# Kernel optimization log

Hardware: AMD Instinct MI355X
Metric: run time of the kernel (lower is better)

Reference implementation:

```python
import jax, jax.numpy as jnp
import numpy as np

H = 512      # hidden_size
GH = 512     # global_hidden_size
V = 128      # VOCAB_SIZE (one-hot arg_hot width)
D = 14       # tree depth; complete binary tree
NUM_OPS = 36
N_INT = 5    # num_internal_ops
N_NODES = 2 ** (D + 1) - 1  # 32767, heap layout: node i has children 2i+1, 2i+2


def _p(key, i, shape, s=0.05):
    return jax.random.normal(jax.random.fold_in(key, i), shape, dtype=jnp.float32) * s


def setup_inputs() -> dict:
    key = jax.random.key(0)
    return {
        "tokens": jax.random.randint(jax.random.fold_in(key, 0), (N_NODES,), 0, V),
        "validity_mask": jnp.ones((NUM_OPS,), jnp.float32),
        # binary tree-LSTM (blstm): 2 children
        "W_iou_b": _p(key, 1, (V, 3 * H)), "U_iou_b": _p(key, 2, (2, H, 3 * H)), "b_iou_b": jnp.zeros((3 * H,), jnp.float32),
        "Wf_b": _p(key, 3, (V, H)), "Uf_b": _p(key, 4, (2, H, H)), "bf_b": jnp.ones((H,), jnp.float32),
        # ternary tree-LSTM (tlstm): 3 children
        "W_iou_t": _p(key, 5, (V, 3 * H)), "U_iou_t": _p(key, 6, (3, H, 3 * H)), "b_iou_t": jnp.zeros((3 * H,), jnp.float32),
        "Wf_t": _p(key, 7, (V, H)), "Uf_t": _p(key, 8, (3, H, H)), "bf_t": jnp.ones((H,), jnp.float32),
        # FFN: one h-by-h layer (ffn_complexity = h^2 * n_layers, n_layers=1)
        "ffn_W": _p(key, 9, (H, H)), "ffn_b": jnp.zeros((H,), jnp.float32),
        # global LSTM (1 layer, 1 step), torch gate order i,f,g,o
        "lstm_Wx": _p(key, 10, (H, 4 * GH)), "lstm_Wh": _p(key, 11, (GH, 4 * GH)), "lstm_b": jnp.zeros((4 * GH,), jnp.float32),
        # actor heads on concat(root_hidden, h_glob)
        "hl_W": _p(key, 12, (H + GH, 2)), "hl_b": jnp.zeros((2,), jnp.float32),
        "int_W": _p(key, 13, (H + GH, N_INT)), "int_b": jnp.zeros((N_INT,), jnp.float32),
        "act_W": _p(key, 14, (H + GH, NUM_OPS)), "act_b": jnp.zeros((NUM_OPS,), jnp.float32),
    }


def _nary_cell(x, hk, ck, W_iou, U_iou, b_iou, Wf, Uf, bf):
    # x: [n, V]; hk, ck: [n, K, H]  (K children)
    iou = x @ W_iou + jnp.einsum('nkh,khg->ng', hk, U_iou) + b_iou
    i, o, u = jnp.split(iou, 3, axis=-1)
    f = jax.nn.sigmoid((x @ Wf + bf)[:, None, :] + jnp.einsum('nkh,khg->nkg', hk, Uf))
    c = jax.nn.sigmoid(i) * jnp.tanh(u) + jnp.sum(f * ck, axis=1)
    h = jax.nn.sigmoid(o) * jnp.tanh(c)
    return h, c


def _forward(tokens, validity_mask, W_iou_b, U_iou_b, b_iou_b, Wf_b, Uf_b, bf_b,
             W_iou_t, U_iou_t, b_iou_t, Wf_t, Uf_t, bf_t, ffn_W, ffn_b,
             lstm_Wx, lstm_Wh, lstm_b, hl_W, hl_b, int_W, int_b, act_W, act_b):
    arg_hot = jax.nn.one_hot(tokens, V, dtype=jnp.float32)  # [N_NODES, V]
    h_prev = c_prev = None
    h_ab = c_ab = None
    # apply_binary_lstm over the whole tree, bottom-up, one batched cell per level
    for lvl in range(D, -1, -1):
        n = 2 ** lvl
        x = arg_hot[n - 1:2 * n - 1]  # level lvl occupies heap slots [2^l-1, 2^{l+1}-2]
        if h_prev is None:
            hk = jnp.zeros((n, 2, H), jnp.float32)  # leaves: tz children
            ck = hk
        else:
            hk = h_prev.reshape(n, 2, H)
            ck = c_prev.reshape(n, 2, H)
        h_prev, c_prev = _nary_cell(x, hk, ck, W_iou_b, U_iou_b, b_iou_b, Wf_b, Uf_b, bf_b)
        if lvl == 1:
            h_ab, c_ab = h_prev, c_prev  # root's children a, b
    # apply_ternary_lstm at depth 0: children = (self.hidden, a.hidden, b.hidden)
    hk3 = jnp.concatenate([h_prev, h_ab], axis=0)[None]  # [1, 3, H]
    ck3 = jnp.concatenate([c_prev, c_ab], axis=0)[None]
    h_root, c_root = _nary_cell(arg_hot[0:1], hk3, ck3, W_iou_t, U_iou_t, b_iou_t, Wf_t, Uf_t, bf_t)
    # apply_ffn (1 layer) then apply_global_lstm (single step from zero state)
    h_f = jnp.maximum(h_root @ ffn_W + ffn_b, 0.0)  # [1, H]
    h_g = jnp.zeros((1, GH), jnp.float32)
    c_g = h_g
    gates = h_f @ lstm_Wx + h_g @ lstm_Wh + lstm_b
    gi, gf, gg, go = jnp.split(gates, 4, axis=-1)
    c_g = jax.nn.sigmoid(gf) * c_g + jax.nn.sigmoid(gi) * jnp.tanh(gg)
    h_g = jax.nn.sigmoid(go) * jnp.tanh(c_g)
    # actor heads
    feat = jnp.concatenate([h_f, h_g], axis=-1)  # [1, H+GH]
    hl = feat @ hl_W + hl_b
    il = feat @ int_W + int_b
    el = jnp.log(validity_mask)[None, :] + feat @ (act_W * validity_mask[None, :]) + act_b * validity_mask
    return jnp.concatenate([hl, il, el], axis=-1)  # [1, 2 + N_INT + NUM_OPS]


def reference(tokens, validity_mask, W_iou_b, U_iou_b, b_iou_b, Wf_b, Uf_b, bf_b,
              W_iou_t, U_iou_t, b_iou_t, Wf_t, Uf_t, bf_t, ffn_W, ffn_b,
              lstm_Wx, lstm_Wh, lstm_b, hl_W, hl_b, int_W, int_b, act_W, act_b):
    return _forward(tokens, validity_mask, W_iou_b, U_iou_b, b_iou_b, Wf_b, Uf_b, bf_b,
                    W_iou_t, U_iou_t, b_iou_t, Wf_t, Uf_t, bf_t, ffn_W, ffn_b,
                    lstm_Wx, lstm_Wh, lstm_b, hl_W, hl_b, int_W, int_b, act_W, act_b)
```

## Files before the change

kernel.cpp:

```cpp
#include <hip/hip_runtime.h>
#include <hip/hip_bf16.h>
#include <math.h>

#define H 512
#define V 128
#define NLEAF 16384

typedef __attribute__((ext_vector_type(4))) float f32x4;
typedef __attribute__((ext_vector_type(8))) short s16x8;
typedef __attribute__((ext_vector_type(4))) unsigned short u16x4;
typedef unsigned short ushort_t;

__device__ ushort_t g_hb0[NLEAF * H];
__device__ ushort_t g_hb1[(NLEAF / 2) * H];
__device__ float    g_c0[NLEAF * H];
__device__ float    g_c1[(NLEAF / 2) * H];
__device__ ushort_t g_UiouT[3 * H * 2 * H];
__device__ ushort_t g_UfT[H * 2 * H];
__device__ ushort_t g_UiouTt[3 * H * 3 * H];
__device__ ushort_t g_UfTt[H * 3 * H];
__device__ float    g_rpart[3 * 3072];
__device__ float    g_root[2 * H];
__device__ float    g_hf[H];
__device__ float    g_gates[4 * H];

__device__ __forceinline__ float sigm(float x) { return 1.0f / (1.0f + __expf(-x)); }
__device__ __forceinline__ float ftanh(float x) {
  return 1.0f - 2.0f / (__expf(2.0f * x) + 1.0f);
}
__device__ __forceinline__ ushort_t f2bf(float x) {
  __hip_bfloat16 b = __float2bfloat16(x);
  return *reinterpret_cast<ushort_t*>(&b);
}
__device__ __forceinline__ float bf2f(ushort_t u) {
  union { unsigned int i; float f; } v; v.i = ((unsigned int)u) << 16; return v.f;
}
__device__ __forceinline__ void gload_lds16(const void* g, void* l) {
  __builtin_amdgcn_global_load_lds(
      (const __attribute__((address_space(1))) unsigned int*)g,
      (__attribute__((address_space(3))) unsigned int*)l, 16, 0, 0);
}

__global__ __launch_bounds__(256) void k_transp(const float* __restrict__ src,
                                                ushort_t* __restrict__ dst,
                                                int R, int Cc) {
  __shared__ float t[32][33];
  int bc = blockIdx.x * 32, br = blockIdx.y * 32;
  int tx = threadIdx.x & 31, ty = threadIdx.x >> 5;
  for (int rr = ty; rr < 32; rr += 8)
    t[rr][tx] = src[(size_t)(br + rr) * Cc + bc + tx];
  __syncthreads();
  for (int rr = ty; rr < 32; rr += 8)
    dst[(size_t)(bc + rr) * R + br + tx] = f2bf(t[tx][rr]);
}

__global__ __launch_bounds__(256) void k_leaf(const int* __restrict__ tokens,
                                              const float* __restrict__ Wiou,
                                              const float* __restrict__ biou) {
  const int total = NLEAF * 128;
  for (int q = blockIdx.x * 256 + threadIdx.x; q < total; q += gridDim.x * 256) {
    int i = q >> 7, jv = q & 127;
    int tok = tokens[(NLEAF - 1) + i];
    const f32x4* Wr = (const f32x4*)(Wiou + (size_t)tok * 1536);
    const f32x4* bv = (const f32x4*)biou;
    f32x4 wi = Wr[jv] + bv[jv];
    f32x4 wo = Wr[128 + jv] + bv[128 + jv];
    f32x4 wu = Wr[256 + jv] + bv[256 + jv];
    u16x4 hv; f32x4 cv;
    #pragma unroll
    for (int r = 0; r < 4; ++r) {
      float c = sigm(wi[r]) * ftanh(wu[r]);
      float h = sigm(wo[r]) * ftanh(c);
      cv[r] = c;
      hv[r] = f2bf(h);
    }
    *reinterpret_cast<u16x4*>(&g_hb0[(size_t)q * 4]) = hv;
    *reinterpret_cast<f32x4*>(&g_c0[(size_t)q * 4]) = cv;
  }
}

__global__ __launch_bounds__(128, 2) void k_mfma_lvl(int lvl,
    const int* __restrict__ tokens,
    const float* __restrict__ Wiou, const float* __restrict__ biou,
    const float* __restrict__ Wf, const float* __restrict__ bf) {
  const int n = 1 << lvl;
  const int node0 = n - 1;
  const int outp = lvl & 1;
  const ushort_t* __restrict__ hprev = outp ? g_hb0 : g_hb1;
  const float* __restrict__ cprev = outp ? g_c0 : g_c1;
  ushort_t* __restrict__ hout = outp ? g_hb1 : g_hb0;
  float* __restrict__ cout = outp ? g_c1 : g_c0;

  const int i0 = blockIdx.x * 64;
  const int j0 = blockIdx.y * 64;
  const int tid = threadIdx.x;
  const int lane = tid & 63;
  const int w = tid >> 6;

  __shared__ f32x4 smemv[2560];
  char* smem = (char*)smemv;

  const char* gp[10];
  unsigned lb[10], lstr[10];
  {
    int kb = (lane >> 4) * 16;
    #pragma unroll
    for (int q = 0; q < 10; ++q) {
      int c = w * 10 + q;
      if (c < 4) {
        int row = i0 + c * 16 + (lane & 15);
        gp[q] = (const char*)hprev + (size_t)row * 2048 + kb;
        lb[q] = c * 1024u;
        lstr[q] = 4096u;
      } else {
        int ct = c - 4;
        int col = ct * 16 + (lane & 15);
        int g = col >> 6, jj = j0 + (col & 63);
        const ushort_t* Ub = (g < 3) ? (g_UiouT + (size_t)(g * 512 + jj) * 1024)
                                     : (g_UfT + (size_t)jj * 1024);
        gp[q] = (const char*)Ub + kb;
        lb[q] = 8192u + ct * 1024u;
        lstr[q] = 16384u;
      }
    }
  }

#define STAGE(BUF)                                                     \
  {                                                                    \
    _Pragma("unroll")                                                  \
    for (int q = 0; q < 10; ++q) {                                     \
      gload_lds16(gp[q], smem + lb[q] + (unsigned)(BUF) * lstr[q]);    \
      gp[q] += 64;                                                     \
    }                                                                  \
  }

  f32x4 acc[4][10];
  #pragma unroll
  for (int a = 0; a < 4; ++a)
    #pragma unroll
    for (int b = 0; b < 10; ++b) acc[a][b] = (f32x4){0.f, 0.f, 0.f, 0.f};

#define COMPUTE(FA)                                                          \
  {                                                                          \
    const char* ab = smem + buf * 4096 + lane * 16;                          \
    s16x8 a0 = *(const s16x8*)(ab);                                          \
    s16x8 a1 = *(const s16x8*)(ab + 1024);                                   \
    s16x8 a2 = *(const s16x8*)(ab + 2048);                                   \
    s16x8 a3 = *(const s16x8*)(ab + 3072);                                   \
    const char* bb = smem + 8192 + buf * 16384 + w * 2048 + lane * 16;       \
    s16x8 b0 = *(const s16x8*)(bb);                                          \
    s16x8 b1 = *(const s16x8*)(bb + 1024);                                   \
    s16x8 b2 = *(const s16x8*)(bb + 4096);                                   \
    s16x8 b3 = *(const s16x8*)(bb + 5120);                                   \
    s16x8 b4 = *(const s16x8*)(bb + 8192);                                   \
    s16x8 b5 = *(const s16x8*)(bb + 9216);                                   \
    s16x8 b6 = *(const s16x8*)(bb + 12288);                                  \
    s16x8 b7 = *(const s16x8*)(bb + 13312);                                  \
    s16x8 aa[4] = {a0, a1, a2, a3};                                          \
    _Pragma("unroll")                                                        \
    for (int rtl = 0; rtl < 4; ++rtl) {                                      \
      acc[rtl][0] = __builtin_amdgcn_mfma_f32_16x16x32_bf16(aa[rtl], b0, acc[rtl][0], 0, 0, 0); \
      acc[rtl][1] = __builtin_amdgcn_mfma_f32_16x16x32_bf16(aa[rtl], b1, acc[rtl][1], 0, 0, 0); \
      acc[rtl][2] = __builtin_amdgcn_mfma_f32_16x16x32_bf16(aa[rtl], b2, acc[rtl][2], 0, 0, 0); \
      acc[rtl][3] = __builtin_amdgcn_mfma_f32_16x16x32_bf16(aa[rtl], b3, acc[rtl][3], 0, 0, 0); \
      acc[rtl][4] = __builtin_amdgcn_mfma_f32_16x16x32_bf16(aa[rtl], b4, acc[rtl][4], 0, 0, 0); \
      acc[rtl][5] = __builtin_amdgcn_mfma_f32_16x16x32_bf16(aa[rtl], b5, acc[rtl][5], 0, 0, 0); \
      acc[rtl][FA] = __builtin_amdgcn_mfma_f32_16x16x32_bf16(aa[rtl], b6, acc[rtl][FA], 0, 0, 0); \
      acc[rtl][FA + 1] = __builtin_amdgcn_mfma_f32_16x16x32_bf16(aa[rtl], b7, acc[rtl][FA + 1], 0, 0, 0); \
    }                                                                        \
  }

  STAGE(0);
  __syncthreads();
  int buf = 0;
  for (int kt = 0; kt < 16; ++kt) {
    STAGE(buf ^ 1);
    COMPUTE(6);
    __syncthreads();
    buf ^= 1;
  }
  for (int kt = 16; kt < 32; ++kt) {
    if (kt < 31) STAGE(buf ^ 1);
    COMPUTE(8);
    __syncthreads();
    buf ^= 1;
  }
#undef COMPUTE
#undef STAGE

  const int node_c = lane >> 4;
  const int jl = lane & 15;
  #pragma unroll
  for (int t = 0; t < 2; ++t) {
    const int j = j0 + w * 32 + t * 16 + jl;
    const float bi = biou[j], bo = biou[512 + j], bu = biou[1024 + j], bfv = bf[j];
    #pragma unroll
    for (int rtl = 0; rtl < 4; ++rtl) {
      f32x4 vi = acc[rtl][0 + t], vo = acc[rtl][2 + t], vu = acc[rtl][4 + t],
            v0 = acc[rtl][6 + t], v1 = acc[rtl][8 + t];
      const int ib = i0 + rtl * 16 + node_c * 4;
      #pragma unroll
      for (int r = 0; r < 4; ++r) {
        int i = ib + r;
        int tok = tokens[node0 + i];
        const float* Wr = Wiou + (size_t)tok * 1536;
        float fpre = Wf[(size_t)tok * 512 + j] + bfv;
        float ig = vi[r] + Wr[j] + bi;
        float og = vo[r] + Wr[512 + j] + bo;
        float ug = vu[r] + Wr[1024 + j] + bu;
        float cc = sigm(ig) * ftanh(ug)
                 + sigm(fpre + v0[r]) * cprev[(size_t)(2 * i) * 512 + j]
                 + sigm(fpre + v1[r]) * cprev[(size_t)(2 * i + 1) * 512 + j];
        float hh = sigm(og) * ftanh(cc);
        hout[(size_t)i * 512 + j] = f2bf(hh);
        cout[(size_t)i * 512 + j] = cc;
      }
    }
  }
}

__global__ __launch_bounds__(256) void k_small(int lvl,
    const int* __restrict__ tokens,
    const float* __restrict__ Wiou, const float* __restrict__ biou,
    const float* __restrict__ Wf, const float* __restrict__ bf) {
  const int n = 1 << lvl;
  const int node0 = n - 1;
  const int outp = lvl & 1;
  const ushort_t* __restrict__ hprev = outp ? g_hb0 : g_hb1;
  const float* __restrict__ cprev = outp ? g_c0 : g_c1;
  ushort_t* __restrict__ hout = outp ? g_hb1 : g_hb0;
  float* __restrict__ cout = outp ? g_c1 : g_c0;

  const int i = blockIdx.y;
  const int j0 = blockIdx.x * 64;
  const int tid = threadIdx.x;
  const int g = tid >> 6;
  const int jc = tid & 63;
  const int jj = j0 + jc;

  __shared__ float hl[1024];
  __shared__ float exch[5][64];
  for (int t = tid; t < 1024; t += 256) hl[t] = bf2f(hprev[(size_t)i * 1024 + t]);
  __syncthreads();

  const ushort_t* col = (g < 3) ? (g_UiouT + (size_t)(g * 512 + jj) * 1024)
                                : (g_UfT + (size_t)jj * 1024);
  float a0 = 0.f, a1 = 0.f;
  #pragma unroll 4
  for (int k0 = 0; k0 < 512; k0 += 8) {
    s16x8 wv = *(const s16x8*)(col + k0);
    #pragma unroll
    for (int r = 0; r < 8; ++r) a0 += hl[k0 + r] * bf2f((ushort_t)wv[r]);
  }
  #pragma unroll 4
  for (int k0 = 512; k0 < 1024; k0 += 8) {
    s16x8 wv = *(const s16x8*)(col + k0);
    #pragma unroll
    for (int r = 0; r < 8; ++r) a1 += hl[k0 + r] * bf2f((ushort_t)wv[r]);
  }
  if (g < 3) exch[g][jc] = a0 + a1;
  else { exch[3][jc] = a0; exch[4][jc] = a1; }
  __syncthreads();

  if (tid < 64) {
    int j = j0 + tid;
    float ai = exch[0][tid], ao = exch[1][tid], au = exch[2][tid];
    float af0 = exch[3][tid], af1 = exch[4][tid];
    int tok = tokens[node0 + i];
    const float* Wr = Wiou + (size_t)tok * 1536;
    float fpre = Wf[(size_t)tok * 512 + j] + bf[j];
    float ig = ai + Wr[j] + biou[j];
    float og = ao + Wr[512 + j] + biou[512 + j];
    float ug = au + Wr[1024 + j] + biou[1024 + j];
    float cc = sigm(ig) * ftanh(ug)
             + sigm(fpre + af0) * cprev[(size_t)(2 * i) * 512 + j]
             + sigm(fpre + af1) * cprev[(size_t)(2 * i + 1) * 512 + j];
    float hh = sigm(og) * ftanh(cc);
    hout[(size_t)i * 512 + j] = f2bf(hh);
    cout[(size_t)i * 512 + j] = cc;
  }
}

__global__ __launch_bounds__(256) void k_root_p1() {
  const int by = blockIdx.y;
  const int tid = threadIdx.x;
  const int c = blockIdx.x * 256 + tid;

  __shared__ float hl[512];
  {
    int m0 = by * 512;
    #pragma unroll
    for (int q = 0; q < 2; ++q) {
      int t = tid + q * 256, m = m0 + t;
      hl[t] = (m < 512) ? bf2f(g_hb0[m]) : bf2f(g_hb1[m - 512]);
    }
  }
  __syncthreads();

  float acc = 0.f;
  const ushort_t* col = nullptr;
  if (c < 1536) {
    col = g_UiouTt + (size_t)c * 1536 + by * 512;
  } else {
    int v = c - 1536;
    if ((v >> 9) == by) col = g_UfTt + (size_t)(v & 511) * 1536 + by * 512;
  }
  if (col) {
    #pragma unroll 4
    for (int k0 = 0; k0 < 512; k0 += 8) {
      s16x8 wv = *(const s16x8*)(col + k0);
      #pragma unroll
      for (int r = 0; r < 8; ++r) acc += hl[k0 + r] * bf2f((ushort_t)wv[r]);
    }
  }
  g_rpart[(size_t)by * 3072 + c] = acc;
}

__global__ __launch_bounds__(512) void k_root_p2(const int* __restrict__ tokens,
    const float* __restrict__ Wiou_t, const float* __restrict__ biou_t,
    const float* __restrict__ Wf_t, const float* __restrict__ bf_t) {
  const int j = threadIdx.x;
  float ai = g_rpart[j] + g_rpart[3072 + j] + g_rpart[6144 + j];
  float ao = g_rpart[512 + j] + g_rpart[3072 + 512 + j] + g_rpart[6144 + 512 + j];
  float au = g_rpart[1024 + j] + g_rpart[3072 + 1024 + j] + g_rpart[6144 + 1024 + j];
  float f0 = g_rpart[1536 + j] + g_rpart[3072 + 1536 + j] + g_rpart[6144 + 1536 + j];
  float f1 = g_rpart[2048 + j] + g_rpart[3072 + 2048 + j] + g_rpart[6144 + 2048 + j];
  float f2 = g_rpart[2560 + j] + g_rpart[3072 + 2560 + j] + g_rpart[6144 + 2560 + j];

  int tok = tokens[0];
  float fpre = Wf_t[(size_t)tok * H + j] + bf_t[j];
  float ig = ai + Wiou_t[(size_t)tok * 3 * H + j] + biou_t[j];
  float og = ao + Wiou_t[(size_t)tok * 3 * H + H + j] + biou_t[H + j];
  float ug = au + Wiou_t[(size_t)tok * 3 * H + 2 * H + j] + biou_t[2 * H + j];
  float cc = sigm(ig) * ftanh(ug)
           + sigm(fpre + f0) * g_c0[j]
           + sigm(fpre + f1) * g_c1[j]
           + sigm(fpre + f2) * g_c1[H + j];
  float hh = sigm(og) * ftanh(cc);
  g_root[j] = hh;
  g_root[H + j] = cc;
}

__global__ __launch_bounds__(512) void k_head1(const float* __restrict__ ffnW,
                                               const float* __restrict__ ffnb) {
  __shared__ float hr[H];
  int j = threadIdx.x;
  hr[j] = g_root[j];
  __syncthreads();
  float acc = ffnb[j];
  #pragma unroll 8
  for (int m = 0; m < H; ++m) acc += hr[m] * ffnW[m * H + j];
  g_hf[j] = fmaxf(acc, 0.0f);
}

__global__ __launch_bounds__(64) void k_head2(const float* __restrict__ Wx,
                                              const float* __restrict__ lb) {
  int g = blockIdx.x * 64 + threadIdx.x;
  float acc = lb[g];
  #pragma unroll 8
  for (int m = 0; m < H; ++m) acc += g_hf[m] * Wx[m * 4 * H + g];
  g_gates[g] = acc;
}

__global__ __launch_bounds__(512) void k_head3(const float* __restrict__ vm,
    const float* __restrict__ hlW, const float* __restrict__ hlb,
    const float* __restrict__ intW, const float* __restrict__ intb,
    const float* __restrict__ actW, const float* __restrict__ actb,
    float* __restrict__ out) {
  __shared__ float feat[2 * H];
  int j = threadIdx.x;
  float ci = sigm(g_gates[j]) * ftanh(g_gates[2 * H + j]);
  float hg = sigm(g_gates[3 * H + j]) * ftanh(ci);
  feat[j] = g_hf[j];
  feat[H + j] = hg;
  __syncthreads();

  const int wv = threadIdx.x >> 6;
  const int lane = threadIdx.x & 63;
  for (int o = wv; o < 43; o += 8) {
    const float* Wc;
    int stride, colb;
    if (o < 2)       { Wc = hlW;  stride = 2;  colb = o; }
    else if (o < 7)  { Wc = intW; stride = 5;  colb = o - 2; }
    else             { Wc = actW; stride = 36; colb = o - 7; }
    float s = 0.f;
    #pragma unroll
    for (int q = 0; q < 16; ++q) {
      int m = lane + q * 64;
      s += feat[m] * Wc[(size_t)m * stride + colb];
    }
    #pragma unroll
    for (int d = 32; d >= 1; d >>= 1) s += __shfl_xor(s, d);
    if (lane == 0) {
      float res;
      if (o < 2)      res = s + hlb[o];
      else if (o < 7) res = s + intb[o - 2];
      else {
        int a = o - 7;
        float v = vm[a];
        res = __logf(v) + s * v + actb[a] * v;
      }
      out[o] = res;
    }
  }
}

extern "C" void kernel_launch(void* const* d_in, const int* in_sizes, int n_in,
                              void* d_out, int out_size, void* d_ws, size_t ws_size,
                              hipStream_t stream) {
  (void)in_sizes; (void)n_in; (void)d_ws; (void)ws_size; (void)out_size;
  const int* tokens   = (const int*)d_in[0];
  const float* vm     = (const float*)d_in[1];
  const float* Wiou_b = (const float*)d_in[2];
  const float* Uiou_b = (const float*)d_in[3];
  const float* biou_b = (const float*)d_in[4];
  const float* Wf_b   = (const float*)d_in[5];
  const float* Uf_b   = (const float*)d_in[6];
  const float* bf_b   = (const float*)d_in[7];
  const float* Wiou_t = (const float*)d_in[8];
  const float* Uiou_t = (const float*)d_in[9];
  const float* biou_t = (const float*)d_in[10];
  const float* Wf_t   = (const float*)d_in[11];
  const float* Uf_t   = (const float*)d_in[12];
  const float* bf_t   = (const float*)d_in[13];
  const float* ffnW   = (const float*)d_in[14];
  const float* ffnb   = (const float*)d_in[15];
  const float* lstmWx = (const float*)d_in[16];
  const float* lstmb  = (const float*)d_in[18];
  const float* hlW    = (const float*)d_in[19];
  const float* hlb    = (const float*)d_in[20];
  const float* intW   = (const float*)d_in[21];
  const float* intb   = (const float*)d_in[22];
  const float* actW   = (const float*)d_in[23];
  const float* actb   = (const float*)d_in[24];

  ushort_t* UiouT;  hipGetSymbolAddress((void**)&UiouT, HIP_SYMBOL(g_UiouT));
  ushort_t* UfT;    hipGetSymbolAddress((void**)&UfT, HIP_SYMBOL(g_UfT));
  ushort_t* UiouTt; hipGetSymbolAddress((void**)&UiouTt, HIP_SYMBOL(g_UiouTt));
  ushort_t* UfTt;   hipGetSymbolAddress((void**)&UfTt, HIP_SYMBOL(g_UfTt));

  k_transp<<<dim3(48, 32), 256, 0, stream>>>(Uiou_b, UiouT, 1024, 1536);
  k_transp<<<dim3(16, 32), 256, 0, stream>>>(Uf_b, UfT, 1024, 512);
  k_transp<<<dim3(48, 48), 256, 0, stream>>>(Uiou_t, UiouTt, 1536, 1536);
  k_transp<<<dim3(16, 48), 256, 0, stream>>>(Uf_t, UfTt, 1536, 512);

  k_leaf<<<2048, 256, 0, stream>>>(tokens, Wiou_b, biou_b);
  for (int lvl = 13; lvl >= 6; --lvl) {
    int gx = (1 << lvl) / 64;
    k_mfma_lvl<<<dim3(gx, 8), 128, 0, stream>>>(lvl, tokens, Wiou_b, biou_b,
                                                Wf_b, bf_b);
  }
  for (int lvl = 5; lvl >= 0; --lvl) {
    int n = 1 << lvl;
    k_small<<<dim3(8, n), 256, 0, stream>>>(lvl, tokens, Wiou_b, biou_b,
                                            Wf_b, bf_b);
  }
  k_root_p1<<<dim3(12, 3), 256, 0, stream>>>();
  k_root_p2<<<1, 512, 0, stream>>>(tokens, Wiou_t, biou_t, Wf_t, bf_t);
  k_head1<<<1, 512, 0, stream>>>(ffnW, ffnb);
  k_head2<<<32, 64, 0, stream>>>(lstmWx, lstmb);
  k_head3<<<1, 512, 0, stream>>>(vm, hlW, hlb, intW, intb, actW, actb, (float*)d_out);
}
```

Measured before the change: 654.2 us.

## Fuse tail levels and heads into persistent kernel with grid barriers; enlarge MFMA tiles

Replaces the per-level small kernels for levels 7..0, the root kernels and the three head kernels with one persistent 256-block kernel that uses atomic grid barriers between stages. This removes about a dozen kernel launches and their gaps. The MFMA level kernel now uses 256 threads and 128-row tiles, so four waves share the B tiles, and it runs only for levels 13..8. The grid barrier relies on all 256 blocks being co-resident, and the two mid-sized levels (7 and 6) move from MFMA to the scalar dot-product path.

```diff
diff --git a/kernel.cpp b/kernel.cpp
--- a/kernel.cpp
+++ b/kernel.cpp
@@ -23,6 +23,7 @@
 __device__ float    g_root[2 * H];
 __device__ float    g_hf[H];
 __device__ float    g_gates[4 * H];
+__device__ unsigned g_bar[64];
 
 __device__ __forceinline__ float sigm(float x) { return 1.0f / (1.0f + __expf(-x)); }
 __device__ __forceinline__ float ftanh(float x) {
@@ -39,6 +40,20 @@
   __builtin_amdgcn_global_load_lds(
       (const __attribute__((address_space(1))) unsigned int*)g,
       (__attribute__((address_space(3))) unsigned int*)l, 16, 0, 0);
+}
+
+#define TAIL_NB 256
+__device__ __forceinline__ void gridbar(int idx) {
+  __threadfence();
+  __syncthreads();
+  if (threadIdx.x == 0) {
+    __hip_atomic_fetch_add(&g_bar[idx], 1u, __ATOMIC_ACQ_REL,
+                           __HIP_MEMORY_SCOPE_AGENT);
+    while (__hip_atomic_load(&g_bar[idx], __ATOMIC_ACQUIRE,
+                             __HIP_MEMORY_SCOPE_AGENT) < TAIL_NB)
+      __builtin_amdgcn_s_sleep(2);
+  }
+  __syncthreads();
 }
 
 __global__ __launch_bounds__(256) void k_transp(const float* __restrict__ src,
@@ -79,7 +94,7 @@
   }
 }
 
-__global__ __launch_bounds__(128, 2) void k_mfma_lvl(int lvl,
+__global__ __launch_bounds__(256, 2) void k_mfma_lvl(int lvl,
     const int* __restrict__ tokens,
     const float* __restrict__ Wiou, const float* __restrict__ biou,
     const float* __restrict__ Wf, const float* __restrict__ bf) {
@@ -91,47 +106,49 @@
   ushort_t* __restrict__ hout = outp ? g_hb1 : g_hb0;
   float* __restrict__ cout = outp ? g_c1 : g_c0;
 
-  const int i0 = blockIdx.x * 64;
+  const int i0 = blockIdx.x * 128;
   const int j0 = blockIdx.y * 64;
   const int tid = threadIdx.x;
   const int lane = tid & 63;
   const int w = tid >> 6;
-
-  __shared__ f32x4 smemv[2560];
+  const int wry = w >> 1;
+  const int cx = w & 1;
+
+  __shared__ f32x4 smemv[3072];
   char* smem = (char*)smemv;
 
-  const char* gp[10];
-  unsigned lb[10], lstr[10];
+  const char* gp[6];
+  unsigned lb[6], lstride[6];
   {
     int kb = (lane >> 4) * 16;
     #pragma unroll
-    for (int q = 0; q < 10; ++q) {
-      int c = w * 10 + q;
-      if (c < 4) {
+    for (int q = 0; q < 6; ++q) {
+      int c = w * 6 + q;
+      if (c < 8) {
         int row = i0 + c * 16 + (lane & 15);
         gp[q] = (const char*)hprev + (size_t)row * 2048 + kb;
         lb[q] = c * 1024u;
-        lstr[q] = 4096u;
+        lstride[q] = 8192u;
       } else {
-        int ct = c - 4;
+        int ct = c - 8;
         int col = ct * 16 + (lane & 15);
         int g = col >> 6, jj = j0 + (col & 63);
         const ushort_t* Ub = (g < 3) ? (g_UiouT + (size_t)(g * 512 + jj) * 1024)
                                      : (g_UfT + (size_t)jj * 1024);
         gp[q] = (const char*)Ub + kb;
-        lb[q] = 8192u + ct * 1024u;
-        lstr[q] = 16384u;
-      }
-    }
-  }
-
-#define STAGE(BUF)                                                     \
-  {                                                                    \
-    _Pragma("unroll")                                                  \
-    for (int q = 0; q < 10; ++q) {                                     \
-      gload_lds16(gp[q], smem + lb[q] + (unsigned)(BUF) * lstr[q]);    \
-      gp[q] += 64;                                                     \
-    }                                                                  \
+        lb[q] = 16384u + ct * 1024u;
+        lstride[q] = 16384u;
+      }
+    }
+  }
+
+#define STAGE(BUF)                                                   \
+  {                                                                  \
+    _Pragma("unroll")                                                \
+    for (int q = 0; q < 6; ++q) {                                    \
+      gload_lds16(gp[q], smem + lb[q] + (unsigned)(BUF) * lstride[q]); \
+      gp[q] += 64;                                                   \
+    }                                                                \
   }
 
   f32x4 acc[4][10];
@@ -142,12 +159,12 @@
 
 #define COMPUTE(FA)                                                          \
   {                                                                          \
-    const char* ab = smem + buf * 4096 + lane * 16;                          \
+    const char* ab = smem + buf * 8192 + wry * 4096 + lane * 16;             \
     s16x8 a0 = *(const s16x8*)(ab);                                          \
     s16x8 a1 = *(const s16x8*)(ab + 1024);                                   \
     s16x8 a2 = *(const s16x8*)(ab + 2048);                                   \
     s16x8 a3 = *(const s16x8*)(ab + 3072);                                   \
-    const char* bb = smem + 8192 + buf * 16384 + w * 2048 + lane * 16;       \
+    const char* bb = smem + 16384 + buf * 16384 + cx * 2048 + lane * 16;     \
     s16x8 b0 = *(const s16x8*)(bb);                                          \
     s16x8 b1 = *(const s16x8*)(bb + 1024);                                   \
     s16x8 b2 = *(const s16x8*)(bb + 4096);                                   \
@@ -192,13 +209,13 @@
   const int jl = lane & 15;
   #pragma unroll
   for (int t = 0; t < 2; ++t) {
-    const int j = j0 + w * 32 + t * 16 + jl;
+    const int j = j0 + cx * 32 + t * 16 + jl;
     const float bi = biou[j], bo = biou[512 + j], bu = biou[1024 + j], bfv = bf[j];
     #pragma unroll
     for (int rtl = 0; rtl < 4; ++rtl) {
       f32x4 vi = acc[rtl][0 + t], vo = acc[rtl][2 + t], vu = acc[rtl][4 + t],
             v0 = acc[rtl][6 + t], v1 = acc[rtl][8 + t];
-      const int ib = i0 + rtl * 16 + node_c * 4;
+      const int ib = i0 + wry * 64 + rtl * 16 + node_c * 4;
       #pragma unroll
       for (int r = 0; r < 4; ++r) {
         int i = ib + r;
@@ -219,188 +236,201 @@
   }
 }
 
-__global__ __launch_bounds__(256) void k_small(int lvl,
+__global__ __launch_bounds__(256, 1) void k_tail(
     const int* __restrict__ tokens,
     const float* __restrict__ Wiou, const float* __restrict__ biou,
-    const float* __restrict__ Wf, const float* __restrict__ bf) {
-  const int n = 1 << lvl;
-  const int node0 = n - 1;
-  const int outp = lvl & 1;
-  const ushort_t* __restrict__ hprev = outp ? g_hb0 : g_hb1;
-  const float* __restrict__ cprev = outp ? g_c0 : g_c1;
-  ushort_t* __restrict__ hout = outp ? g_hb1 : g_hb0;
-  float* __restrict__ cout = outp ? g_c1 : g_c0;
-
-  const int i = blockIdx.y;
-  const int j0 = blockIdx.x * 64;
-  const int tid = threadIdx.x;
-  const int g = tid >> 6;
-  const int jc = tid & 63;
-  const int jj = j0 + jc;
-
-  __shared__ float hl[1024];
-  __shared__ float exch[5][64];
-  for (int t = tid; t < 1024; t += 256) hl[t] = bf2f(hprev[(size_t)i * 1024 + t]);
-  __syncthreads();
-
-  const ushort_t* col = (g < 3) ? (g_UiouT + (size_t)(g * 512 + jj) * 1024)
-                                : (g_UfT + (size_t)jj * 1024);
-  float a0 = 0.f, a1 = 0.f;
-  #pragma unroll 4
-  for (int k0 = 0; k0 < 512; k0 += 8) {
-    s16x8 wv = *(const s16x8*)(col + k0);
-    #pragma unroll
-    for (int r = 0; r < 8; ++r) a0 += hl[k0 + r] * bf2f((ushort_t)wv[r]);
-  }
-  #pragma unroll 4
-  for (int k0 = 512; k0 < 1024; k0 += 8) {
-    s16x8 wv = *(const s16x8*)(col + k0);
-    #pragma unroll
-    for (int r = 0; r < 8; ++r) a1 += hl[k0 + r] * bf2f((ushort_t)wv[r]);
-  }
-  if (g < 3) exch[g][jc] = a0 + a1;
-  else { exch[3][jc] = a0; exch[4][jc] = a1; }
-  __syncthreads();
-
-  if (tid < 64) {
-    int j = j0 + tid;
-    float ai = exch[0][tid], ao = exch[1][tid], au = exch[2][tid];
-    float af0 = exch[3][tid], af1 = exch[4][tid];
-    int tok = tokens[node0 + i];
-    const float* Wr = Wiou + (size_t)tok * 1536;
-    float fpre = Wf[(size_t)tok * 512 + j] + bf[j];
-    float ig = ai + Wr[j] + biou[j];
-    float og = ao + Wr[512 + j] + biou[512 + j];
-    float ug = au + Wr[1024 + j] + biou[1024 + j];
-    float cc = sigm(ig) * ftanh(ug)
-             + sigm(fpre + af0) * cprev[(size_t)(2 * i) * 512 + j]
-             + sigm(fpre + af1) * cprev[(size_t)(2 * i + 1) * 512 + j];
-    float hh = sigm(og) * ftanh(cc);
-    hout[(size_t)i * 512 + j] = f2bf(hh);
-    cout[(size_t)i * 512 + j] = cc;
-  }
-}
-
-__global__ __launch_bounds__(256) void k_root_p1() {
-  const int by = blockIdx.y;
-  const int tid = threadIdx.x;
-  const int c = blockIdx.x * 256 + tid;
-
-  __shared__ float hl[512];
-  {
-    int m0 = by * 512;
-    #pragma unroll
-    for (int q = 0; q < 2; ++q) {
-      int t = tid + q * 256, m = m0 + t;
-      hl[t] = (m < 512) ? bf2f(g_hb0[m]) : bf2f(g_hb1[m - 512]);
-    }
-  }
-  __syncthreads();
-
-  float acc = 0.f;
-  const ushort_t* col = nullptr;
-  if (c < 1536) {
-    col = g_UiouTt + (size_t)c * 1536 + by * 512;
-  } else {
-    int v = c - 1536;
-    if ((v >> 9) == by) col = g_UfTt + (size_t)(v & 511) * 1536 + by * 512;
-  }
-  if (col) {
-    #pragma unroll 4
-    for (int k0 = 0; k0 < 512; k0 += 8) {
-      s16x8 wv = *(const s16x8*)(col + k0);
-      #pragma unroll
-      for (int r = 0; r < 8; ++r) acc += hl[k0 + r] * bf2f((ushort_t)wv[r]);
-    }
-  }
-  g_rpart[(size_t)by * 3072 + c] = acc;
-}
-
-__global__ __launch_bounds__(512) void k_root_p2(const int* __restrict__ tokens,
+    const float* __restrict__ Wf, const float* __restrict__ bf,
     const float* __restrict__ Wiou_t, const float* __restrict__ biou_t,
-    const float* __restrict__ Wf_t, const float* __restrict__ bf_t) {
-  const int j = threadIdx.x;
-  float ai = g_rpart[j] + g_rpart[3072 + j] + g_rpart[6144 + j];
-  float ao = g_rpart[512 + j] + g_rpart[3072 + 512 + j] + g_rpart[6144 + 512 + j];
-  float au = g_rpart[1024 + j] + g_rpart[3072 + 1024 + j] + g_rpart[6144 + 1024 + j];
-  float f0 = g_rpart[1536 + j] + g_rpart[3072 + 1536 + j] + g_rpart[6144 + 1536 + j];
-  float f1 = g_rpart[2048 + j] + g_rpart[3072 + 2048 + j] + g_rpart[6144 + 2048 + j];
-  float f2 = g_rpart[2560 + j] + g_rpart[3072 + 2560 + j] + g_rpart[6144 + 2560 + j];
-
-  int tok = tokens[0];
-  float fpre = Wf_t[(size_t)tok * H + j] + bf_t[j];
-  float ig = ai + Wiou_t[(size_t)tok * 3 * H + j] + biou_t[j];
-  float og = ao + Wiou_t[(size_t)tok * 3 * H + H + j] + biou_t[H + j];
-  float ug = au + Wiou_t[(size_t)tok * 3 * H + 2 * H + j] + biou_t[2 * H + j];
-  float cc = sigm(ig) * ftanh(ug)
-           + sigm(fpre + f0) * g_c0[j]
-           + sigm(fpre + f1) * g_c1[j]
-           + sigm(fpre + f2) * g_c1[H + j];
-  float hh = sigm(og) * ftanh(cc);
-  g_root[j] = hh;
-  g_root[H + j] = cc;
-}
-
-__global__ __launch_bounds__(512) void k_head1(const float* __restrict__ ffnW,
-                                               const float* __restrict__ ffnb) {
-  __shared__ float hr[H];
-  int j = threadIdx.x;
-  hr[j] = g_root[j];
-  __syncthreads();
-  float acc = ffnb[j];
-  #pragma unroll 8
-  for (int m = 0; m < H; ++m) acc += hr[m] * ffnW[m * H + j];
-  g_hf[j] = fmaxf(acc, 0.0f);
-}
-
-__global__ __launch_bounds__(64) void k_head2(const float* __restrict__ Wx,
-                                              const float* __restrict__ lb) {
-  int g = blockIdx.x * 64 + threadIdx.x;
-  float acc = lb[g];
-  #pragma unroll 8
-  for (int m = 0; m < H; ++m) acc += g_hf[m] * Wx[m * 4 * H + g];
-  g_gates[g] = acc;
-}
-
-__global__ __launch_bounds__(512) void k_head3(const float* __restrict__ vm,
+    const float* __restrict__ Wf_t, const float* __restrict__ bf_t,
+    const float* __restrict__ ffnW, const float* __restrict__ ffnb,
+    const float* __restrict__ Wx, const float* __restrict__ lb,
+    const float* __restrict__ vm,
     const float* __restrict__ hlW, const float* __restrict__ hlb,
     const float* __restrict__ intW, const float* __restrict__ intb,
     const float* __restrict__ actW, const float* __restrict__ actb,
     float* __restrict__ out) {
-  __shared__ float feat[2 * H];
-  int j = threadIdx.x;
-  float ci = sigm(g_gates[j]) * ftanh(g_gates[2 * H + j]);
-  float hg = sigm(g_gates[3 * H + j]) * ftanh(ci);
-  feat[j] = g_hf[j];
-  feat[H + j] = hg;
-  __syncthreads();
-
-  const int wv = threadIdx.x >> 6;
-  const int lane = threadIdx.x & 63;
-  for (int o = wv; o < 43; o += 8) {
-    const float* Wc;
-    int stride, colb;
-    if (o < 2)       { Wc = hlW;  stride = 2;  colb = o; }
-    else if (o < 7)  { Wc = intW; stride = 5;  colb = o - 2; }
-    else             { Wc = actW; stride = 36; colb = o - 7; }
-    float s = 0.f;
+  __shared__ float hl[1024];
+  __shared__ float exch[5][64];
+  const int b = blockIdx.x;
+  const int tid = threadIdx.x;
+  int barid = 0;
+
+  for (int lvl = 7; lvl >= 0; --lvl) {
+    const int n = 1 << lvl;
+    const int node0 = n - 1;
+    const int outp = lvl & 1;
+    const ushort_t* __restrict__ hprev = outp ? g_hb0 : g_hb1;
+    const float* __restrict__ cprev = outp ? g_c0 : g_c1;
+    ushort_t* __restrict__ hout = outp ? g_hb1 : g_hb0;
+    float* __restrict__ cout = outp ? g_c1 : g_c0;
+    const int tasks = 8 * n;
+    for (int t = b; t < tasks; t += TAIL_NB) {
+      const int i = t >> 3;
+      const int j0 = (t & 7) * 64;
+      const int g = tid >> 6;
+      const int jc = tid & 63;
+      const int jj = j0 + jc;
+      __syncthreads();
+      for (int q = tid; q < 1024; q += 256)
+        hl[q] = bf2f(hprev[(size_t)i * 1024 + q]);
+      __syncthreads();
+
+      const ushort_t* col = (g < 3) ? (g_UiouT + (size_t)(g * 512 + jj) * 1024)
+                                    : (g_UfT + (size_t)jj * 1024);
+      float a0 = 0.f, a1 = 0.f;
+      #pragma unroll 4
+      for (int k0 = 0; k0 < 512; k0 += 8) {
+        s16x8 wv = *(const s16x8*)(col + k0);
+        #pragma unroll
+        for (int r = 0; r < 8; ++r) a0 += hl[k0 + r] * bf2f((ushort_t)wv[r]);
+      }
+      #pragma unroll 4
+      for (int k0 = 512; k0 < 1024; k0 += 8) {
+        s16x8 wv = *(const s16x8*)(col + k0);
+        #pragma unroll
+        for (int r = 0; r < 8; ++r) a1 += hl[k0 + r] * bf2f((ushort_t)wv[r]);
+      }
+      if (g < 3) exch[g][jc] = a0 + a1;
+      else { exch[3][jc] = a0; exch[4][jc] = a1; }
+      __syncthreads();
+
+      if (tid < 64) {
+        int j = j0 + tid;
+        float ai = exch[0][tid], ao = exch[1][tid], au = exch[2][tid];
+        float af0 = exch[3][tid], af1 = exch[4][tid];
+        int tok = tokens[node0 + i];
+        const float* Wr = Wiou + (size_t)tok * 1536;
+        float fpre = Wf[(size_t)tok * 512 + j] + bf[j];
+        float ig = ai + Wr[j] + biou[j];
+        float og = ao + Wr[512 + j] + biou[512 + j];
+        float ug = au + Wr[1024 + j] + biou[1024 + j];
+        float cc = sigm(ig) * ftanh(ug)
+                 + sigm(fpre + af0) * cprev[(size_t)(2 * i) * 512 + j]
+                 + sigm(fpre + af1) * cprev[(size_t)(2 * i + 1) * 512 + j];
+        float hh = sigm(og) * ftanh(cc);
+        hout[(size_t)i * 512 + j] = f2bf(hh);
+        cout[(size_t)i * 512 + j] = cc;
+      }
+    }
+    gridbar(barid++);
+  }
+
+  if (b < 36) {
+    const int by = b / 12;
+    const int cc = (b % 12) * 256 + tid;
+    __syncthreads();
+    {
+      int m0 = by * 512;
+      for (int q = tid; q < 512; q += 256) {
+        int m = m0 + q;
+        hl[q] = (m < 512) ? bf2f(g_hb0[m]) : bf2f(g_hb1[m - 512]);
+      }
+    }
+    __syncthreads();
+    float acc = 0.f;
+    const ushort_t* col = nullptr;
+    if (cc < 1536) {
+      col = g_UiouTt + (size_t)cc * 1536 + by * 512;
+    } else {
+      int v = cc - 1536;
+      if ((v >> 9) == by) col = g_UfTt + (size_t)(v & 511) * 1536 + by * 512;
+    }
+    if (col) {
+      #pragma unroll 4
+      for (int k0 = 0; k0 < 512; k0 += 8) {
+        s16x8 wv = *(const s16x8*)(col + k0);
+        #pragma unroll
+        for (int r = 0; r < 8; ++r) acc += hl[k0 + r] * bf2f((ushort_t)wv[r]);
+      }
+    }
+    g_rpart[(size_t)by * 3072 + cc] = acc;
+  }
+  gridbar(barid++);
+
+  if (b < 2) {
+    int j = b * 256 + tid;
+    float ai = g_rpart[j] + g_rpart[3072 + j] + g_rpart[6144 + j];
+    float ao = g_rpart[512 + j] + g_rpart[3072 + 512 + j] + g_rpart[6144 + 512 + j];
+    float au = g_rpart[1024 + j] + g_rpart[3072 + 1024 + j] + g_rpart[6144 + 1024 + j];
+    float f0 = g_rpart[1536 + j] + g_rpart[3072 + 1536 + j] + g_rpart[6144 + 1536 + j];
+    float f1 = g_rpart[2048 + j] + g_rpart[3072 + 2048 + j] + g_rpart[6144 + 2048 + j];
+    float f2 = g_rpart[2560 + j] + g_rpart[3072 + 2560 + j] + g_rpart[6144 + 2560 + j];
+    int tok = tokens[0];
+    float fpre = Wf_t[(size_t)tok * 512 + j] + bf_t[j];
+    float ig = ai + Wiou_t[(size_t)tok * 1536 + j] + biou_t[j];
+    float og = ao + Wiou_t[(size_t)tok * 1536 + 512 + j] + biou_t[512 + j];
+    float ug = au + Wiou_t[(size_t)tok * 1536 + 1024 + j] + biou_t[1024 + j];
+    float cc = sigm(ig) * ftanh(ug)
+             + sigm(fpre + f0) * g_c0[j]
+             + sigm(fpre + f1) * g_c1[j]
+             + sigm(fpre + f2) * g_c1[512 + j];
+    float hh = sigm(og) * ftanh(cc);
+    g_root[j] = hh;
+    g_root[512 + j] = cc;
+  }
+  gridbar(barid++);
+
+  if (b < 2) {
+    int j = b * 256 + tid;
+    __syncthreads();
+    for (int q = tid; q < 512; q += 256) hl[q] = g_root[q];
+    __syncthreads();
+    float acc = ffnb[j];
+    #pragma unroll 8
+    for (int m = 0; m < 512; ++m) acc += hl[m] * ffnW[m * 512 + j];
+    g_hf[j] = fmaxf(acc, 0.0f);
+  }
+  gridbar(barid++);
+
+  if (b < 8) {
+    int g2 = b * 256 + tid;
+    __syncthreads();
+    for (int q = tid; q < 512; q += 256) hl[q] = g_hf[q];
+    __syncthreads();
+    float acc = lb[g2];
+    #pragma unroll 8
+    for (int m = 0; m < 512; ++m) acc += hl[m] * Wx[m * 2048 + g2];
+    g_gates[g2] = acc;
+  }
+  gridbar(barid++);
+
+  if (b == 0) {
     #pragma unroll
-    for (int q = 0; q < 16; ++q) {
-      int m = lane + q * 64;
-      s += feat[m] * Wc[(size_t)m * stride + colb];
-    }
-    #pragma unroll
-    for (int d = 32; d >= 1; d >>= 1) s += __shfl_xor(s, d);
-    if (lane == 0) {
-      float res;
-      if (o < 2)      res = s + hlb[o];
-      else if (o < 7) res = s + intb[o - 2];
-      else {
-        int a = o - 7;
-        float v = vm[a];
-        res = __logf(v) + s * v + actb[a] * v;
-      }
-      out[o] = res;
+    for (int q = 0; q < 2; ++q) {
+      int j = tid + q * 256;
+      float ci = sigm(g_gates[j]) * ftanh(g_gates[1024 + j]);
+      float hg = sigm(g_gates[1536 + j]) * ftanh(ci);
+      hl[j] = g_hf[j];
+      hl[512 + j] = hg;
+    }
+    __syncthreads();
+    const int wv = tid >> 6;
+    const int lane = tid & 63;
+    for (int o = wv; o < 43; o += 4) {
+      const float* Wc;
+      int stride, colb;
+      if (o < 2)       { Wc = hlW;  stride = 2;  colb = o; }
+      else if (o < 7)  { Wc = intW; stride = 5;  colb = o - 2; }
+      else             { Wc = actW; stride = 36; colb = o - 7; }
+      float s = 0.f;
+      #pragma unroll
+      for (int q = 0; q < 16; ++q) {
+        int m = lane + q * 64;
+        s += hl[m] * Wc[(size_t)m * stride + colb];
+      }
+      #pragma unroll
+      for (int d = 32; d >= 1; d >>= 1) s += __shfl_xor(s, d);
+      if (lane == 0) {
+        float res;
+        if (o < 2)      res = s + hlb[o];
+        else if (o < 7) res = s + intb[o - 2];
+        else {
+          int a = o - 7;
+          float v = vm[a];
+          res = __logf(v) + s * v + actb[a] * v;
+        }
+        out[o] = res;
+      }
     }
   }
 }
@@ -438,6 +468,9 @@
   ushort_t* UfT;    hipGetSymbolAddress((void**)&UfT, HIP_SYMBOL(g_UfT));
   ushort_t* UiouTt; hipGetSymbolAddress((void**)&UiouTt, HIP_SYMBOL(g_UiouTt));
   ushort_t* UfTt;   hipGetSymbolAddress((void**)&UfTt, HIP_SYMBOL(g_UfTt));
+  unsigned* barp;   hipGetSymbolAddress((void**)&barp, HIP_SYMBOL(g_bar));
+
+  hipMemsetAsync(barp, 0, 64 * sizeof(unsigned), stream);
 
   k_transp<<<dim3(48, 32), 256, 0, stream>>>(Uiou_b, UiouT, 1024, 1536);
   k_transp<<<dim3(16, 32), 256, 0, stream>>>(Uf_b, UfT, 1024, 512);
@@ -445,19 +478,14 @@
   k_transp<<<dim3(16, 48), 256, 0, stream>>>(Uf_t, UfTt, 1536, 512);
 
   k_leaf<<<2048, 256, 0, stream>>>(tokens, Wiou_b, biou_b);
-  for (int lvl = 13; lvl >= 6; --lvl) {
-    int gx = (1 << lvl) / 64;
-    k_mfma_lvl<<<dim3(gx, 8), 128, 0, stream>>>(lvl, tokens, Wiou_b, biou_b,
+  for (int lvl = 13; lvl >= 8; --lvl) {
+    int gx = (1 << lvl) / 128;
+    k_mfma_lvl<<<dim3(gx, 8), 256, 0, stream>>>(lvl, tokens, Wiou_b, biou_b,
                                                 Wf_b, bf_b);
   }
-  for (int lvl = 5; lvl >= 0; --lvl) {
-    int n = 1 << lvl;
-    k_small<<<dim3(8, n), 256, 0, stream>>>(lvl, tokens, Wiou_b, biou_b,
-                                            Wf_b, bf_b);
-  }
-  k_root_p1<<<dim3(12, 3), 256, 0, stream>>>();
-  k_root_p2<<<1, 512, 0, stream>>>(tokens, Wiou_t, biou_t, Wf_t, bf_t);
-  k_head1<<<1, 512, 0, stream>>>(ffnW, ffnb);
-  k_head2<<<32, 64, 0, stream>>>(lstmWx, lstmb);
-  k_head3<<<1, 512, 0, stream>>>(vm, hlW, hlb, intW, intb, actW, actb, (float*)d_out);
-}
+  k_tail<<<TAIL_NB, 256, 0, stream>>>(tokens, Wiou_b, biou_b, Wf_b, bf_b,
+                                      Wiou_t, biou_t, Wf_t, bf_t,
+                                      ffnW, ffnb, lstmWx, lstmb, vm,
+                                      hlW, hlb, intW, intb, actW, actb,
+                                      (float*)d_out);
+}
```

After: 1.754 ms. +168.1%, slower.

## Enlarge MFMA level tiles to 128 nodes, merge transpose launches, extend small path

Applied to the files above, without the earlier changes.

The per-level MFMA kernel now uses 256 threads and covers 128 tree nodes per block. Four waves are arranged 2x2, so each U-weight tile loaded into LDS serves twice as many nodes, which halves weight traffic per node. The four weight-transpose launches are merged into one grid with a z dimension and early exit for out-of-range blocks. Levels 6 and 7 move to the k_small path because the bigger tile would leave too few blocks there. The costs are fewer blocks in flight per level and possibly slower k_small handling of the wider levels.

```diff
diff --git a/kernel.cpp b/kernel.cpp
--- a/kernel.cpp
+++ b/kernel.cpp
@@ -41,11 +41,21 @@
       (__attribute__((address_space(3))) unsigned int*)l, 16, 0, 0);
 }
 
-__global__ __launch_bounds__(256) void k_transp(const float* __restrict__ src,
-                                                ushort_t* __restrict__ dst,
-                                                int R, int Cc) {
+__global__ __launch_bounds__(256) void k_transp_all(
+    const float* __restrict__ s0, const float* __restrict__ s1,
+    const float* __restrict__ s2, const float* __restrict__ s3,
+    ushort_t* __restrict__ d0, ushort_t* __restrict__ d1,
+    ushort_t* __restrict__ d2, ushort_t* __restrict__ d3) {
+  const float* src; ushort_t* dst; int R, Cc;
+  switch (blockIdx.z) {
+    case 0: src = s0; dst = d0; R = 1024; Cc = 1536; break;
+    case 1: src = s1; dst = d1; R = 1024; Cc = 512; break;
+    case 2: src = s2; dst = d2; R = 1536; Cc = 1536; break;
+    default: src = s3; dst = d3; R = 1536; Cc = 512; break;
+  }
+  int bc = blockIdx.x * 32, br = blockIdx.y * 32;
+  if (bc >= Cc || br >= R) return;
   __shared__ float t[32][33];
-  int bc = blockIdx.x * 32, br = blockIdx.y * 32;
   int tx = threadIdx.x & 31, ty = threadIdx.x >> 5;
   for (int rr = ty; rr < 32; rr += 8)
     t[rr][tx] = src[(size_t)(br + rr) * Cc + bc + tx];
@@ -79,7 +89,7 @@
   }
 }
 
-__global__ __launch_bounds__(128, 2) void k_mfma_lvl(int lvl,
+__global__ __launch_bounds__(256, 2) void k_mfma_lvl(int lvl,
     const int* __restrict__ tokens,
     const float* __restrict__ Wiou, const float* __restrict__ biou,
     const float* __restrict__ Wf, const float* __restrict__ bf) {
@@ -91,47 +101,49 @@
   ushort_t* __restrict__ hout = outp ? g_hb1 : g_hb0;
   float* __restrict__ cout = outp ? g_c1 : g_c0;
 
-  const int i0 = blockIdx.x * 64;
+  const int i0 = blockIdx.x * 128;
   const int j0 = blockIdx.y * 64;
   const int tid = threadIdx.x;
   const int lane = tid & 63;
   const int w = tid >> 6;
-
-  __shared__ f32x4 smemv[2560];
+  const int wry = w >> 1;
+  const int cx = w & 1;
+
+  __shared__ f32x4 smemv[3072];
   char* smem = (char*)smemv;
 
-  const char* gp[10];
-  unsigned lb[10], lstr[10];
+  const char* gp[6];
+  unsigned lb[6], lstride[6];
   {
     int kb = (lane >> 4) * 16;
     #pragma unroll
-    for (int q = 0; q < 10; ++q) {
-      int c = w * 10 + q;
-      if (c < 4) {
+    for (int q = 0; q < 6; ++q) {
+      int c = w * 6 + q;
+      if (c < 8) {
         int row = i0 + c * 16 + (lane & 15);
         gp[q] = (const char*)hprev + (size_t)row * 2048 + kb;
         lb[q] = c * 1024u;
-        lstr[q] = 4096u;
+        lstride[q] = 8192u;
       } else {
-        int ct = c - 4;
+        int ct = c - 8;
         int col = ct * 16 + (lane & 15);
         int g = col >> 6, jj = j0 + (col & 63);
         const ushort_t* Ub = (g < 3) ? (g_UiouT + (size_t)(g * 512 + jj) * 1024)
                                      : (g_UfT + (size_t)jj * 1024);
         gp[q] = (const char*)Ub + kb;
-        lb[q] = 8192u + ct * 1024u;
-        lstr[q] = 16384u;
+        lb[q] = 16384u + ct * 1024u;
+        lstride[q] = 16384u;
       }
     }
   }
 
-#define STAGE(BUF)                                                     \
-  {                                                                    \
-    _Pragma("unroll")                                                  \
-    for (int q = 0; q < 10; ++q) {                                     \
-      gload_lds16(gp[q], smem + lb[q] + (unsigned)(BUF) * lstr[q]);    \
-      gp[q] += 64;                                                     \
-    }                                                                  \
+#define STAGE(BUF)                                                   \
+  {                                                                  \
+    _Pragma("unroll")                                                \
+    for (int q = 0; q < 6; ++q) {                                    \
+      gload_lds16(gp[q], smem + lb[q] + (unsigned)(BUF) * lstride[q]); \
+      gp[q] += 64;                                                   \
+    }                                                                \
   }
 
   f32x4 acc[4][10];
@@ -142,12 +154,12 @@
 
 #define COMPUTE(FA)                                                          \
   {                                                                          \
-    const char* ab = smem + buf * 4096 + lane * 16;                          \
+    const char* ab = smem + buf * 8192 + wry * 4096 + lane * 16;             \
     s16x8 a0 = *(const s16x8*)(ab);                                          \
     s16x8 a1 = *(const s16x8*)(ab + 1024);                                   \
     s16x8 a2 = *(const s16x8*)(ab + 2048);                                   \
     s16x8 a3 = *(const s16x8*)(ab + 3072);                                   \
-    const char* bb = smem + 8192 + buf * 16384 + w * 2048 + lane * 16;       \
+    const char* bb = smem + 16384 + buf * 16384 + cx * 2048 + lane * 16;     \
     s16x8 b0 = *(const s16x8*)(bb);                                          \
     s16x8 b1 = *(const s16x8*)(bb + 1024);                                   \
     s16x8 b2 = *(const s16x8*)(bb + 4096);                                   \
@@ -192,13 +204,13 @@
   const int jl = lane & 15;
   #pragma unroll
   for (int t = 0; t < 2; ++t) {
-    const int j = j0 + w * 32 + t * 16 + jl;
+    const int j = j0 + cx * 32 + t * 16 + jl;
     const float bi = biou[j], bo = biou[512 + j], bu = biou[1024 + j], bfv = bf[j];
     #pragma unroll
     for (int rtl = 0; rtl < 4; ++rtl) {
       f32x4 vi = acc[rtl][0 + t], vo = acc[rtl][2 + t], vu = acc[rtl][4 + t],
             v0 = acc[rtl][6 + t], v1 = acc[rtl][8 + t];
-      const int ib = i0 + rtl * 16 + node_c * 4;
+      const int ib = i0 + wry * 64 + rtl * 16 + node_c * 4;
       #pragma unroll
       for (int r = 0; r < 4; ++r) {
         int i = ib + r;
@@ -439,18 +451,16 @@
   ushort_t* UiouTt; hipGetSymbolAddress((void**)&UiouTt, HIP_SYMBOL(g_UiouTt));
   ushort_t* UfTt;   hipGetSymbolAddress((void**)&UfTt, HIP_SYMBOL(g_UfTt));
 
-  k_transp<<<dim3(48, 32), 256, 0, stream>>>(Uiou_b, UiouT, 1024, 1536);
-  k_transp<<<dim3(16, 32), 256, 0, stream>>>(Uf_b, UfT, 1024, 512);
-  k_transp<<<dim3(48, 48), 256, 0, stream>>>(Uiou_t, UiouTt, 1536, 1536);
-  k_transp<<<dim3(16, 48), 256, 0, stream>>>(Uf_t, UfTt, 1536, 512);
+  k_transp_all<<<dim3(48, 48, 4), 256, 0, stream>>>(
+      Uiou_b, Uf_b, Uiou_t, Uf_t, UiouT, UfT, UiouTt, UfTt);
 
   k_leaf<<<2048, 256, 0, stream>>>(tokens, Wiou_b, biou_b);
-  for (int lvl = 13; lvl >= 6; --lvl) {
-    int gx = (1 << lvl) / 64;
-    k_mfma_lvl<<<dim3(gx, 8), 128, 0, stream>>>(lvl, tokens, Wiou_b, biou_b,
+  for (int lvl = 13; lvl >= 8; --lvl) {
+    int gx = (1 << lvl) / 128;
+    k_mfma_lvl<<<dim3(gx, 8), 256, 0, stream>>>(lvl, tokens, Wiou_b, biou_b,
                                                 Wf_b, bf_b);
   }
-  for (int lvl = 5; lvl >= 0; --lvl) {
+  for (int lvl = 7; lvl >= 0; --lvl) {
     int n = 1 << lvl;
     k_small<<<dim3(8, n), 256, 0, stream>>>(lvl, tokens, Wiou_b, biou_b,
                                             Wf_b, bf_b);
```

Measured after the change: 658.6 us. Within noise of the previous version (+0.7%).
